# Performance work log

Measured on AMD Instinct MI355X. Metric: run time of the kernel, lower is better.

Reference implementation:

```python
import jax, jax.numpy as jnp
import numpy as np

DIM = 1024
N_HEADS = 8
N_KV_HEADS = 8
Q_C = 128
Q_NOPE = 96
Q_ROPE = 32
KV_C = 128
K_NOPE = 64
K_ROPE = 64
V_HD = 256
EPS = 1e-8
ROPE_THETA = 10000.0


def rms_norm(x, w, eps=EPS):
    return w * x * jax.lax.rsqrt(jnp.mean(x * x, axis=-1, keepdims=True) + eps)


def apply_rope(x, position_ids, head_dim):
    # x: [B, H, S, hd], interleaved even/odd rotation (matches torch module)
    inv_freq = 1.0 / (ROPE_THETA ** (jnp.arange(0, head_dim, 2, dtype=jnp.float32) / head_dim))
    ang = position_ids.astype(jnp.float32)[:, None, :, None] * inv_freq  # [B,1,S,hd/2]
    cos, sin = jnp.cos(ang), jnp.sin(ang)
    xe, xo = x[..., ::2], x[..., 1::2]
    rot = jnp.stack((xe * cos - xo * sin, xe * sin + xo * cos), axis=-1)
    return rot.reshape(x.shape)


def setup_inputs() -> dict:
    key = jax.random.key(0)
    ks = jax.random.split(key, 12)
    B, S = 2, 2048
    s = 0.02
    return {
        "x": jax.random.normal(ks[0], (B, S, DIM), jnp.float32),
        "position_ids": jnp.broadcast_to(jnp.arange(S, dtype=jnp.int32), (B, S)),
        "w_dq_w": jax.random.normal(ks[1], (DIM, Q_C), jnp.float32) * s,
        "w_dq_b": jnp.zeros((Q_C,), jnp.float32),
        "q_norm_w": jnp.ones((Q_C,), jnp.float32),
        "w_uq_qr_w": jax.random.normal(ks[2], (Q_C, N_HEADS * (Q_NOPE + Q_ROPE)), jnp.float32) * s,
        "w_uq_qr_b": jnp.zeros((N_HEADS * (Q_NOPE + Q_ROPE),), jnp.float32),
        "w_dkv_kr_w": jax.random.normal(ks[3], (DIM, KV_C + K_ROPE), jnp.float32) * s,
        "w_dkv_kr_b": jnp.zeros((KV_C + K_ROPE,), jnp.float32),
        "kv_norm_w": jnp.ones((KV_C,), jnp.float32),
        "w_uk_uv_w": jax.random.normal(ks[4], (KV_C, N_KV_HEADS * (K_NOPE + V_HD)), jnp.float32) * s,
        "w_uk_uv_b": jnp.zeros((N_KV_HEADS * (K_NOPE + V_HD),), jnp.float32),
        "w_o_w": jax.random.normal(ks[5], (N_HEADS * V_HD, DIM), jnp.float32) * s,
        "w_o_b": jnp.zeros((DIM,), jnp.float32),
    }


def reference(x, position_ids, w_dq_w, w_dq_b, q_norm_w, w_uq_qr_w, w_uq_qr_b,
              w_dkv_kr_w, w_dkv_kr_b, kv_norm_w, w_uk_uv_w, w_uk_uv_b, w_o_w, w_o_b):
    B, S, _ = x.shape
    # --- Q path: compress -> norm -> up-project, split nope/rope ---
    cq = rms_norm(x @ w_dq_w + w_dq_b, q_norm_w)                     # [B,S,Qc]
    q = cq @ w_uq_qr_w + w_uq_qr_b                                   # [B,S,H*(96+32)]
    q_nope, q_rope = jnp.split(q, [N_HEADS * Q_NOPE], axis=-1)
    q_nope = q_nope.reshape(B, S, N_HEADS, Q_NOPE).transpose(0, 2, 1, 3)
    q_rope = q_rope.reshape(B, S, N_HEADS, Q_ROPE).transpose(0, 2, 1, 3)
    q_rope = apply_rope(q_rope, position_ids, Q_ROPE)
    q_states = jnp.concatenate((q_nope, q_rope), axis=-1)            # [B,H,S,128]
    # --- KV path: compress + shared rope key ---
    ckv_kr = x @ w_dkv_kr_w + w_dkv_kr_b
    ckv, k_rope = jnp.split(ckv_kr, [KV_C], axis=-1)
    ckv = rms_norm(ckv, kv_norm_w)                                   # [B,S,KVc]
    k_rope = apply_rope(k_rope[:, None, :, :], position_ids, K_ROPE) # [B,1,S,64]
    kv = ckv @ w_uk_uv_w + w_uk_uv_b                                 # [B,S,KVh*(64+256)]
    k_nope, v = jnp.split(kv, [N_KV_HEADS * K_NOPE], axis=-1)
    k_nope = k_nope.reshape(B, S, N_KV_HEADS, K_NOPE).transpose(0, 2, 1, 3)
    k_rope = jnp.broadcast_to(k_rope, (B, N_KV_HEADS, S, K_ROPE))
    k_states = jnp.concatenate((k_nope, k_rope), axis=-1)            # [B,KVh,S,128]
    v_states = v.reshape(B, S, N_KV_HEADS, V_HD).transpose(0, 2, 1, 3)
    # gqa_factor = n_heads // n_kv_heads = 1 -> repeat is a no-op
    # --- SDPA (no mask), scale = 1/sqrt(q head dim) ---
    scale = 1.0 / jnp.sqrt(jnp.float32(Q_NOPE + Q_ROPE))
    scores = jnp.einsum("bhqd,bhkd->bhqk", q_states, k_states) * scale
    probs = jax.nn.softmax(scores, axis=-1)
    attn = jnp.einsum("bhqk,bhkd->bhqd", probs, v_states)            # [B,H,S,256]
    attn = attn.transpose(0, 2, 1, 3).reshape(B, S, N_HEADS * V_HD)
    return attn @ w_o_w + w_o_b
```

## Files before the change

kernel.cpp:

```cpp
#include <hip/hip_runtime.h>
#include <hip/hip_bf16.h>
#include <stdint.h>

typedef unsigned short u16;
typedef short short8 __attribute__((ext_vector_type(8)));
typedef float floatx4 __attribute__((ext_vector_type(4)));

#define S_LEN 2048
#define NB 2
#define NH 8
#define R_TOK (NB * S_LEN)

#define L2_THETA 13.287712379549449f
#define QSCALE (0.08838834764831845f * 1.4426950408889634f)

__device__ inline u16 f2bf(float f) {
  union { float f; uint32_t u; } x; x.f = f;
  uint32_t r = (x.u + 0x7fffu + ((x.u >> 16) & 1u)) >> 16;
  return (u16)r;
}
__device__ inline float bf2f(u16 h) {
  union { uint32_t u; float f; } x; x.u = ((uint32_t)h) << 16;
  return x.f;
}
__device__ inline floatx4 mfma16(short8 a, short8 b, floatx4 c) {
  return __builtin_amdgcn_mfma_f32_16x16x32_bf16(a, b, c, 0, 0, 0);
}
__device__ inline uint32_t pkbf(float a, float b) {
  union { __hip_bfloat162 h; uint32_t u; } c;
  c.h = __float22bfloat162_rn(make_float2(a, b));
  return c.u;
}
__device__ __forceinline__ void cp16(const void* g, const void* l) {
  __builtin_amdgcn_global_load_lds(
      (const __attribute__((address_space(1))) uint32_t*)(uintptr_t)g,
      (__attribute__((address_space(3))) uint32_t*)(uintptr_t)l, 16, 0, 0);
}

__global__ __launch_bounds__(256) void k_prep(
    const float* __restrict__ x, u16* __restrict__ xbf,
    const float* __restrict__ wdq, const float* __restrict__ wdkv, u16* __restrict__ waT,
    const float* __restrict__ wuq, u16* __restrict__ wQT,
    const float* __restrict__ wukv, u16* __restrict__ wKVT,
    const float* __restrict__ wo, u16* __restrict__ wOT,
    const float* __restrict__ bdq, const float* __restrict__ bdkv,
    float* __restrict__ biasA) {
  __shared__ u16 tile[32][33];
  const int s = blockIdx.x, tid = threadIdx.x;
  const int tx = tid & 31, ty = tid >> 5;
  if (s < 4096) {
    int i = s * 256 + tid;
    float4 v = ((const float4*)x)[i];
    ushort4 o;
    o.x = f2bf(v.x); o.y = f2bf(v.y); o.z = f2bf(v.z); o.w = f2bf(v.w);
    ((ushort4*)xbf)[i] = o;
  } else if (s < 4416) {
    int t = s - 4096, bx = t % 10, by = t / 10;
    int c0 = bx * 32, r0 = by * 32;
#pragma unroll
    for (int i = 0; i < 4; ++i) {
      int r = r0 + ty + i * 8, c = c0 + tx;
      float v = (c < 128) ? wdq[(size_t)r * 128 + c] : wdkv[(size_t)r * 192 + (c - 128)];
      tile[ty + i * 8][tx] = f2bf(v);
    }
    __syncthreads();
#pragma unroll
    for (int i = 0; i < 4; ++i)
      waT[(size_t)(c0 + ty + i * 8) * 1024 + r0 + tx] = tile[tx][ty + i * 8];
  } else {
    const float* in; u16* out; int R, C, bx, by;
    if (s < 4544) { int t = s - 4416; in = wuq; out = wQT; R = 128; C = 1024; bx = t & 31; by = t >> 5; }
    else if (s < 4864) { int t = s - 4544; in = wukv; out = wKVT; R = 128; C = 2560; bx = t % 80; by = t / 80; }
    else if (s < 6912) { int t = s - 4864; in = wo; out = wOT; R = 2048; C = 1024; bx = t & 31; by = t >> 5; }
    else {
      if (tid < 320) biasA[tid] = (tid < 128) ? bdq[tid] : bdkv[tid - 128];
      return;
    }
    int c0 = bx * 32, r0 = by * 32;
#pragma unroll
    for (int i = 0; i < 4; ++i)
      tile[ty + i * 8][tx] = f2bf(in[(size_t)(r0 + ty + i * 8) * C + c0 + tx]);
    __syncthreads();
#pragma unroll
    for (int i = 0; i < 4; ++i)
      out[(size_t)(c0 + ty + i * 8) * R + r0 + tx] = tile[tx][ty + i * 8];
  }
}

template <int OUT_BF>
__global__ __launch_bounds__(256) void k_gemm_bt(const u16* __restrict__ A,
                                                 const u16* __restrict__ BT,
                                                 const float* __restrict__ bias,
                                                 void* __restrict__ Cout,
                                                 int M, int N, int K) {
  __shared__ __align__(16) u16 Alds[2][128 * 32];
  __shared__ __align__(16) u16 Blds[2][128 * 32];
  const int tid = threadIdx.x;
  const int wave = tid >> 6, lane = tid & 63;
  const int lane15 = lane & 15, quad = lane >> 4;
  const int m0 = blockIdx.y * 128, n0 = blockIdx.x * 128;
  const int mw = (wave & 1) * 64, nw = (wave >> 1) * 64;

  floatx4 acc[4][4];
#pragma unroll
  for (int a = 0; a < 4; ++a)
#pragma unroll
    for (int b = 0; b < 4; ++b) acc[a][b] = (floatx4){0.f, 0.f, 0.f, 0.f};

  const int srow = wave * 32 + (lane >> 2);
  const int scol = (lane & 3) * 8;

  auto stage = [&](int k0, int buf) {
    const u16* ga = A + (size_t)(m0 + srow) * K + k0 + scol;
    cp16(ga, Alds[buf] + srow * 32 + scol);
    cp16(ga + (size_t)16 * K, Alds[buf] + (srow + 16) * 32 + scol);
    const u16* gb = BT + (size_t)(n0 + srow) * K + k0 + scol;
    cp16(gb, Blds[buf] + srow * 32 + scol);
    cp16(gb + (size_t)16 * K, Blds[buf] + (srow + 16) * 32 + scol);
  };

  stage(0, 0);
  int cur = 0;
  for (int k0 = 0; k0 < K; k0 += 32) {
    __syncthreads();
    if (k0 + 32 < K) stage(k0 + 32, cur ^ 1);
    short8 af[4], bf[4];
#pragma unroll
    for (int im = 0; im < 4; ++im)
      af[im] = *(const short8*)&Alds[cur][(mw + im * 16 + lane15) * 32 + quad * 8];
#pragma unroll
    for (int in = 0; in < 4; ++in)
      bf[in] = *(const short8*)&Blds[cur][(nw + in * 16 + lane15) * 32 + quad * 8];
#pragma unroll
    for (int im = 0; im < 4; ++im)
#pragma unroll
      for (int in = 0; in < 4; ++in) acc[im][in] = mfma16(af[im], bf[in], acc[im][in]);
    cur ^= 1;
  }

#pragma unroll
  for (int im = 0; im < 4; ++im)
#pragma unroll
    for (int in = 0; in < 4; ++in)
#pragma unroll
      for (int r = 0; r < 4; ++r) {
        int row = m0 + mw + im * 16 + quad * 4 + r;
        int col = n0 + nw + in * 16 + lane15;
        if (col < N) {
          float v = acc[im][in][r] + bias[col];
          if (OUT_BF)
            ((u16*)Cout)[(size_t)row * N + col] = f2bf(v);
          else
            ((float*)Cout)[(size_t)row * N + col] = v;
        }
      }
}

__global__ void k_stagea(const float* __restrict__ t0, const float* __restrict__ qnw,
                         const float* __restrict__ kvnw, const int* __restrict__ pos_ids,
                         u16* __restrict__ cq, u16* __restrict__ ckv,
                         u16* __restrict__ krope) {
  int r = blockIdx.x, tid = threadIdx.x;
  const float* row = t0 + (size_t)r * 320;
  float a = row[tid];
  float b = row[128 + tid];
  float sa = a * a, sb = b * b;
#pragma unroll
  for (int d = 1; d < 64; d <<= 1) {
    sa += __shfl_xor(sa, d);
    sb += __shfl_xor(sb, d);
  }
  __shared__ float red[4];
  if ((tid & 63) == 0) { red[(tid >> 6) * 2] = sa; red[(tid >> 6) * 2 + 1] = sb; }
  __syncthreads();
  sa = red[0] + red[2];
  sb = red[1] + red[3];
  float ra = rsqrtf(sa * (1.0f / 128.0f) + 1e-8f);
  float rb = rsqrtf(sb * (1.0f / 128.0f) + 1e-8f);
  cq[(size_t)r * 128 + tid] = f2bf(qnw[tid] * a * ra);
  ckv[(size_t)r * 128 + tid] = f2bf(kvnw[tid] * b * rb);
  if (tid < 32) {
    float xe = row[256 + 2 * tid], xo = row[256 + 2 * tid + 1];
    float p = (float)pos_ids[r];
    float freq = exp2f(-(2.0f * tid / 64.0f) * L2_THETA);
    float ang = p * freq;
    float c = cosf(ang), s = sinf(ang);
    krope[(size_t)r * 64 + 2 * tid] = f2bf(xe * c - xo * s);
    krope[(size_t)r * 64 + 2 * tid + 1] = f2bf(xe * s + xo * c);
  }
}

__global__ void k_stageb(const u16* __restrict__ q, const int* __restrict__ pos_ids,
                         u16* __restrict__ qstates) {
  int r = blockIdx.x, tid = threadIdx.x;
  int b = r >> 11, s = r & (S_LEN - 1);
  float p = (float)pos_ids[r];
#pragma unroll
  for (int i = 0; i < 4; ++i) {
    int idx = tid + i * 256;
    int h = idx >> 7, d = idx & 127;
    float val;
    if (d < 96) {
      val = bf2f(q[(size_t)r * 1024 + h * 96 + d]);
    } else {
      int j = d - 96, pr = j >> 1;
      float xe = bf2f(q[(size_t)r * 1024 + 768 + h * 32 + 2 * pr]);
      float xo = bf2f(q[(size_t)r * 1024 + 768 + h * 32 + 2 * pr + 1]);
      float freq = exp2f(-(2.0f * pr / 32.0f) * L2_THETA);
      float ang = p * freq;
      float c = cosf(ang), sn = sinf(ang);
      val = (j & 1) ? (xe * sn + xo * c) : (xe * c - xo * sn);
    }
    qstates[((size_t)(b * NH + h) * S_LEN + s) * 128 + d] = f2bf(val * QSCALE);
  }
}

__global__ __launch_bounds__(256) void k_vt(const u16* __restrict__ kvb, u16* __restrict__ vT) {
  __shared__ u16 tile[64][40];
  const int nx = blockIdx.x;
  const int sy = blockIdx.y;
  const int pz = blockIdx.z;
  const int b = pz >> 3, h = pz & 7;
  const int tid = threadIdx.x;
  const int n0 = nx * 32, s0 = sy * 64;
  {
    int rr = tid >> 2, cc = (tid & 3) * 8;
    const u16* src = kvb + ((size_t)(b * S_LEN + s0 + rr)) * 2560 + 512 + h * 256 + n0 + cc;
    *(short8*)&tile[rr][cc] = *(const short8*)src;
  }
  __syncthreads();
#pragma unroll
  for (int j = 0; j < 2; ++j) {
    int e = tid * 2 + j;
    int n = e >> 4, a = e & 15;
    int sb = 32 * (a >> 3) + 16 * (a & 1) + 4 * ((a >> 1) & 3);
    ushort4 o;
    o.x = tile[sb][n]; o.y = tile[sb + 1][n]; o.z = tile[sb + 2][n]; o.w = tile[sb + 3][n];
    *(ushort4*)&vT[((size_t)(pz * 256 + n0 + n)) * 2048 + s0 + a * 4] = o;
  }
}

__global__ __launch_bounds__(512) void k_attn(const u16* __restrict__ qstates,
                                              const u16* __restrict__ kv,
                                              const u16* __restrict__ krope,
                                              const u16* __restrict__ vT,
                                              u16* __restrict__ attn_out) {
  const int pair = blockIdx.x;
  const int qblk = blockIdx.y;
  const int b = pair >> 3, h = pair & 7;
  const int tid = threadIdx.x;
  const int wave = tid >> 6, lane = tid & 63;
  const int lane15 = lane & 15, quad = lane >> 4;
  const int w4 = wave & 3, half = wave >> 2;

  __shared__ __align__(16) u16 Klds[2][64 * 128];
  __shared__ __align__(16) u16 Vlds[2][256 * 64];

  const int qrow0 = qblk * 128 + wave * 16;
  short8 qfrag[4];
  {
    const u16* qb = qstates + ((size_t)(b * NH + h) * S_LEN + qrow0 + lane15) * 128 + quad * 8;
#pragma unroll
    for (int c = 0; c < 4; ++c) qfrag[c] = *(const short8*)(qb + c * 32);
  }

  floatx4 o_acc[16];
#pragma unroll
  for (int g = 0; g < 16; ++g) o_acc[g] = (floatx4){0.f, 0.f, 0.f, 0.f};
  float m_i = -1e30f;
  float l_i = 0.f;

  const int kbase = (quad * 16 + lane15) * 8;
  int vo0[4], vo1[4];
#pragma unroll
  for (int ph = 0; ph < 4; ++ph) {
    int n = ph * 16 + lane15;
    int sw = (n ^ (n >> 3)) & 7;
    vo0[ph] = n * 64 + ((quad ^ sw) & 7) * 8;
    vo1[ph] = n * 64 + (((quad | 4) ^ sw) & 7) * 8;
  }

  const u16* kp[2];
  int kstr[2];
  int kdst[2];
#pragma unroll
  for (int j = 0; j < 2; ++j) {
    int u = half * 8 + j * 4 + quad;
    const u16* base;
    int str;
    if (u < 8) { base = kv + h * 64 + u * 8; str = 2560; }
    else { base = krope + (u - 8) * 8; str = 64; }
    kp[j] = base + (size_t)(b * S_LEN + w4 * 16 + lane15) * str;
    kstr[j] = str;
    kdst[j] = (w4 * 256 + (half * 2 + j) * 64 + lane) * 8;
  }
  const int vn6 = tid >> 3, vsl = tid & 7;
  const u16* vp[4];
#pragma unroll
  for (int oi = 0; oi < 4; ++oi) {
    int n = oi * 64 + vn6;
    int u = vsl ^ ((n ^ (n >> 3)) & 7);
    vp[oi] = vT + ((size_t)pair * 256 + n) * 2048 + u * 8;
  }

  auto issueK = [&](int buf) {
#pragma unroll
    for (int j = 0; j < 2; ++j) {
      cp16(kp[j], &Klds[buf][kdst[j]]);
      kp[j] += (size_t)64 * kstr[j];
    }
  };
  auto issueV = [&](int buf) {
#pragma unroll
    for (int oi = 0; oi < 4; ++oi) {
      cp16(vp[oi], &Vlds[buf][(oi * 512 + tid) * 8]);
      vp[oi] += 64;
    }
  };

  issueK(0);
  issueV(0);
  asm volatile("s_waitcnt vmcnt(0)" ::: "memory");
  __builtin_amdgcn_sched_barrier(0);
  __builtin_amdgcn_s_barrier();

  int cur = 0;
  for (int ch = 0; ch < S_LEN / 64; ++ch) {
    if (ch + 1 < S_LEN / 64) {
      issueK(cur ^ 1);
      issueV(cur ^ 1);
    }

    floatx4 st[4];
#pragma unroll
    for (int t = 0; t < 4; ++t) st[t] = (floatx4){0.f, 0.f, 0.f, 0.f};
    __builtin_amdgcn_s_setprio(1);
#pragma unroll
    for (int c = 0; c < 4; ++c) {
      short8 qf = qfrag[c];
#pragma unroll
      for (int t = 0; t < 4; ++t) {
        short8 kf = *(const short8*)&Klds[cur][kbase + (t * 16 + c * 4) * 128];
        st[t] = mfma16(kf, qf, st[t]);
      }
    }
    __builtin_amdgcn_s_setprio(0);

    float mloc = st[0][0];
#pragma unroll
    for (int t = 0; t < 4; ++t)
#pragma unroll
      for (int r = 0; r < 4; ++r) mloc = fmaxf(mloc, st[t][r]);
    mloc = fmaxf(mloc, __shfl_xor(mloc, 16));
    mloc = fmaxf(mloc, __shfl_xor(mloc, 32));

    const bool resc = __any(mloc > m_i + 8.0f);
    const float mref = resc ? fmaxf(m_i, mloc) : m_i;

    float rs = 0.f;
    union { short8 s; uint4 u; } a01, a23;
    {
      float p0, p1, p2, p3;
      p0 = exp2f(st[0][0] - mref); p1 = exp2f(st[0][1] - mref);
      p2 = exp2f(st[0][2] - mref); p3 = exp2f(st[0][3] - mref);
      rs += (p0 + p1) + (p2 + p3);
      a01.u.x = pkbf(p0, p1); a01.u.y = pkbf(p2, p3);
      p0 = exp2f(st[1][0] - mref); p1 = exp2f(st[1][1] - mref);
      p2 = exp2f(st[1][2] - mref); p3 = exp2f(st[1][3] - mref);
      rs += (p0 + p1) + (p2 + p3);
      a01.u.z = pkbf(p0, p1); a01.u.w = pkbf(p2, p3);
      p0 = exp2f(st[2][0] - mref); p1 = exp2f(st[2][1] - mref);
      p2 = exp2f(st[2][2] - mref); p3 = exp2f(st[2][3] - mref);
      rs += (p0 + p1) + (p2 + p3);
      a23.u.x = pkbf(p0, p1); a23.u.y = pkbf(p2, p3);
      p0 = exp2f(st[3][0] - mref); p1 = exp2f(st[3][1] - mref);
      p2 = exp2f(st[3][2] - mref); p3 = exp2f(st[3][3] - mref);
      rs += (p0 + p1) + (p2 + p3);
      a23.u.z = pkbf(p0, p1); a23.u.w = pkbf(p2, p3);
    }

    if (resc) {
      float alpha = exp2f(m_i - mref);
      m_i = mref;
      l_i = l_i * alpha + rs;
      float al[4];
#pragma unroll
      for (int r = 0; r < 4; ++r) al[r] = __shfl(alpha, quad * 4 + r, 16);
#pragma unroll
      for (int g = 0; g < 16; ++g) {
        o_acc[g][0] *= al[0]; o_acc[g][1] *= al[1];
        o_acc[g][2] *= al[2]; o_acc[g][3] *= al[3];
      }
    } else {
      l_i += rs;
    }

    __builtin_amdgcn_s_setprio(1);
#pragma unroll
    for (int g = 0; g < 16; ++g) {
      short8 b01 = *(const short8*)&Vlds[cur][vo0[g & 3] + (g >> 2) * 4096];
      short8 b23 = *(const short8*)&Vlds[cur][vo1[g & 3] + (g >> 2) * 4096];
      floatx4 o = o_acc[g];
      o = mfma16(a01.s, b01, o);
      o = mfma16(a23.s, b23, o);
      o_acc[g] = o;
    }
    __builtin_amdgcn_s_setprio(0);

    asm volatile("s_waitcnt vmcnt(0)" ::: "memory");
    __builtin_amdgcn_sched_barrier(0);
    __builtin_amdgcn_s_barrier();
    cur ^= 1;
  }

  float lsum = l_i;
  lsum += __shfl_xor(lsum, 16);
  lsum += __shfl_xor(lsum, 32);
  float rl = 1.0f / lsum;
  float linv[4];
#pragma unroll
  for (int r = 0; r < 4; ++r) linv[r] = __shfl(rl, quad * 4 + r, 16);
#pragma unroll
  for (int g = 0; g < 16; ++g) {
#pragma unroll
    for (int r = 0; r < 4; ++r) {
      int row = qrow0 + quad * 4 + r;
      int col = h * 256 + g * 16 + lane15;
      attn_out[((size_t)b * S_LEN + row) * 2048 + col] = f2bf(o_acc[g][r] * linv[r]);
    }
  }
}

extern "C" void kernel_launch(void* const* d_in, const int* in_sizes, int n_in,
                              void* d_out, int out_size, void* d_ws, size_t ws_size,
                              hipStream_t stream) {
  const float* x = (const float*)d_in[0];
  const int* pos = (const int*)d_in[1];
  const float* wdq = (const float*)d_in[2];
  const float* bdq = (const float*)d_in[3];
  const float* qnw = (const float*)d_in[4];
  const float* wuq = (const float*)d_in[5];
  const float* buq = (const float*)d_in[6];
  const float* wdkv = (const float*)d_in[7];
  const float* bdkv = (const float*)d_in[8];
  const float* kvnw = (const float*)d_in[9];
  const float* wukv = (const float*)d_in[10];
  const float* bukv = (const float*)d_in[11];
  const float* wo = (const float*)d_in[12];
  const float* bo = (const float*)d_in[13];
  float* out = (float*)d_out;

  char* ws = (char*)d_ws;
  size_t off = 0;
  auto alloc = [&](size_t bytes) {
    char* p = ws + off;
    off += (bytes + 255) & ~(size_t)255;
    return p;
  };
  u16* xbf = (u16*)alloc((size_t)R_TOK * 1024 * 2);
  float* t0 = (float*)alloc((size_t)R_TOK * 320 * 4);
  u16* qout = (u16*)alloc((size_t)R_TOK * 1024 * 2);
  u16* vT = (u16*)d_ws;
  u16* waT = (u16*)alloc((size_t)384 * 1024 * 2);
  float* biasA = (float*)alloc(320 * 4);
  u16* wQT = (u16*)alloc((size_t)1024 * 128 * 2);
  u16* wKVT = (u16*)alloc((size_t)2560 * 128 * 2);
  u16* wOT = (u16*)alloc((size_t)1024 * 2048 * 2);
  u16* cq = (u16*)alloc((size_t)R_TOK * 128 * 2);
  u16* ckv = (u16*)alloc((size_t)R_TOK * 128 * 2);
  u16* krope = (u16*)alloc((size_t)R_TOK * 64 * 2);
  u16* qst = (u16*)alloc((size_t)R_TOK * 1024 * 2);
  u16* kvb = (u16*)alloc((size_t)R_TOK * 2560 * 2);
  u16* attnb = (u16*)alloc((size_t)R_TOK * 2048 * 2);
  (void)ws_size; (void)n_in; (void)in_sizes; (void)out_size;

  k_prep<<<6913, 256, 0, stream>>>(x, xbf, wdq, wdkv, waT, wuq, wQT, wukv, wKVT, wo, wOT,
                                   bdq, bdkv, biasA);

  k_gemm_bt<0><<<dim3(3, 32), 256, 0, stream>>>(xbf, waT, biasA, t0, R_TOK, 320, 1024);
  k_stagea<<<R_TOK, 128, 0, stream>>>(t0, qnw, kvnw, pos, cq, ckv, krope);
  k_gemm_bt<1><<<dim3(8, 32), 256, 0, stream>>>(cq, wQT, buq, qout, R_TOK, 1024, 128);
  k_stageb<<<R_TOK, 256, 0, stream>>>(qout, pos, qst);
  k_gemm_bt<1><<<dim3(20, 32), 256, 0, stream>>>(ckv, wKVT, bukv, kvb, R_TOK, 2560, 128);
  k_vt<<<dim3(8, 32, 16), 256, 0, stream>>>(kvb, vT);
  k_attn<<<dim3(16, 16), 512, 0, stream>>>(qst, kvb, krope, vT, attnb);
  k_gemm_bt<0><<<dim3(8, 32), 256, 0, stream>>>(attnb, wOT, bo, out, R_TOK, 1024, 2048);
}
```

Measured before the change: 275.0 us.

## Split attention waves into query-pair by V-half tiles for operand reuse

Each wave now handles two 16-row query slices and half of the 256-wide V output instead of one 16-row slice over all 256 columns. Each K fragment read from LDS feeds two MFMAs and each V fragment feeds two, roughly halving LDS read traffic per MFMA. The cost is that QK^T scores and softmax are computed twice, once in each V-half wave. Launch bounds also request 2 blocks per CU, which constrains registers; with 512-thread blocks and 64 KB LDS each, that target may also be tight on shared memory.

```diff
diff --git a/kernel.cpp b/kernel.cpp
--- a/kernel.cpp
+++ b/kernel.cpp
@@ -240,35 +240,40 @@
   }
 }
 
-__global__ __launch_bounds__(512) void k_attn(const u16* __restrict__ qstates,
-                                              const u16* __restrict__ kv,
-                                              const u16* __restrict__ krope,
-                                              const u16* __restrict__ vT,
-                                              u16* __restrict__ attn_out) {
+__global__ __launch_bounds__(512, 2) void k_attn(const u16* __restrict__ qstates,
+                                                 const u16* __restrict__ kv,
+                                                 const u16* __restrict__ krope,
+                                                 const u16* __restrict__ vT,
+                                                 u16* __restrict__ attn_out) {
   const int pair = blockIdx.x;
   const int qblk = blockIdx.y;
   const int b = pair >> 3, h = pair & 7;
   const int tid = threadIdx.x;
   const int wave = tid >> 6, lane = tid & 63;
   const int lane15 = lane & 15, quad = lane >> 4;
-  const int w4 = wave & 3, half = wave >> 2;
+  const int qg = wave & 3;
+  const int nh = wave >> 2;
 
   __shared__ __align__(16) u16 Klds[2][64 * 128];
   __shared__ __align__(16) u16 Vlds[2][256 * 64];
 
-  const int qrow0 = qblk * 128 + wave * 16;
-  short8 qfrag[4];
-  {
-    const u16* qb = qstates + ((size_t)(b * NH + h) * S_LEN + qrow0 + lane15) * 128 + quad * 8;
-#pragma unroll
-    for (int c = 0; c < 4; ++c) qfrag[c] = *(const short8*)(qb + c * 32);
-  }
-
-  floatx4 o_acc[16];
-#pragma unroll
-  for (int g = 0; g < 16; ++g) o_acc[g] = (floatx4){0.f, 0.f, 0.f, 0.f};
-  float m_i = -1e30f;
-  float l_i = 0.f;
+  const int qrow0 = qblk * 128 + qg * 32;
+  short8 qfrag[2][4];
+#pragma unroll
+  for (int s = 0; s < 2; ++s) {
+    const u16* qb =
+        qstates + ((size_t)(b * NH + h) * S_LEN + qrow0 + s * 16 + lane15) * 128 + quad * 8;
+#pragma unroll
+    for (int c = 0; c < 4; ++c) qfrag[s][c] = *(const short8*)(qb + c * 32);
+  }
+
+  floatx4 o_acc[2][8];
+#pragma unroll
+  for (int s = 0; s < 2; ++s)
+#pragma unroll
+    for (int g = 0; g < 8; ++g) o_acc[s][g] = (floatx4){0.f, 0.f, 0.f, 0.f};
+  float m_i[2] = {-1e30f, -1e30f};
+  float l_i[2] = {0.f, 0.f};
 
   const int kbase = (quad * 16 + lane15) * 8;
   int vo0[4], vo1[4];
@@ -276,8 +281,8 @@
   for (int ph = 0; ph < 4; ++ph) {
     int n = ph * 16 + lane15;
     int sw = (n ^ (n >> 3)) & 7;
-    vo0[ph] = n * 64 + ((quad ^ sw) & 7) * 8;
-    vo1[ph] = n * 64 + (((quad | 4) ^ sw) & 7) * 8;
+    vo0[ph] = nh * 8192 + n * 64 + ((quad ^ sw) & 7) * 8;
+    vo1[ph] = nh * 8192 + n * 64 + (((quad | 4) ^ sw) & 7) * 8;
   }
 
   const u16* kp[2];
@@ -285,14 +290,14 @@
   int kdst[2];
 #pragma unroll
   for (int j = 0; j < 2; ++j) {
-    int u = half * 8 + j * 4 + quad;
+    int u = nh * 8 + j * 4 + quad;
     const u16* base;
     int str;
     if (u < 8) { base = kv + h * 64 + u * 8; str = 2560; }
     else { base = krope + (u - 8) * 8; str = 64; }
-    kp[j] = base + (size_t)(b * S_LEN + w4 * 16 + lane15) * str;
+    kp[j] = base + (size_t)(b * S_LEN + qg * 16 + lane15) * str;
     kstr[j] = str;
-    kdst[j] = (w4 * 256 + (half * 2 + j) * 64 + lane) * 8;
+    kdst[j] = (qg * 256 + (nh * 2 + j) * 64 + lane) * 8;
   }
   const int vn6 = tid >> 3, vsl = tid & 7;
   const u16* vp[4];
@@ -331,79 +336,84 @@
       issueV(cur ^ 1);
     }
 
-    floatx4 st[4];
-#pragma unroll
-    for (int t = 0; t < 4; ++t) st[t] = (floatx4){0.f, 0.f, 0.f, 0.f};
+    floatx4 st[2][4];
+#pragma unroll
+    for (int s = 0; s < 2; ++s)
+#pragma unroll
+      for (int t = 0; t < 4; ++t) st[s][t] = (floatx4){0.f, 0.f, 0.f, 0.f};
     __builtin_amdgcn_s_setprio(1);
 #pragma unroll
     for (int c = 0; c < 4; ++c) {
-      short8 qf = qfrag[c];
 #pragma unroll
       for (int t = 0; t < 4; ++t) {
         short8 kf = *(const short8*)&Klds[cur][kbase + (t * 16 + c * 4) * 128];
-        st[t] = mfma16(kf, qf, st[t]);
+        st[0][t] = mfma16(kf, qfrag[0][c], st[0][t]);
+        st[1][t] = mfma16(kf, qfrag[1][c], st[1][t]);
       }
     }
     __builtin_amdgcn_s_setprio(0);
 
-    float mloc = st[0][0];
-#pragma unroll
-    for (int t = 0; t < 4; ++t)
-#pragma unroll
-      for (int r = 0; r < 4; ++r) mloc = fmaxf(mloc, st[t][r]);
-    mloc = fmaxf(mloc, __shfl_xor(mloc, 16));
-    mloc = fmaxf(mloc, __shfl_xor(mloc, 32));
-
-    const bool resc = __any(mloc > m_i + 8.0f);
-    const float mref = resc ? fmaxf(m_i, mloc) : m_i;
-
-    float rs = 0.f;
-    union { short8 s; uint4 u; } a01, a23;
-    {
-      float p0, p1, p2, p3;
-      p0 = exp2f(st[0][0] - mref); p1 = exp2f(st[0][1] - mref);
-      p2 = exp2f(st[0][2] - mref); p3 = exp2f(st[0][3] - mref);
-      rs += (p0 + p1) + (p2 + p3);
-      a01.u.x = pkbf(p0, p1); a01.u.y = pkbf(p2, p3);
-      p0 = exp2f(st[1][0] - mref); p1 = exp2f(st[1][1] - mref);
-      p2 = exp2f(st[1][2] - mref); p3 = exp2f(st[1][3] - mref);
-      rs += (p0 + p1) + (p2 + p3);
-      a01.u.z = pkbf(p0, p1); a01.u.w = pkbf(p2, p3);
-      p0 = exp2f(st[2][0] - mref); p1 = exp2f(st[2][1] - mref);
-      p2 = exp2f(st[2][2] - mref); p3 = exp2f(st[2][3] - mref);
-      rs += (p0 + p1) + (p2 + p3);
-      a23.u.x = pkbf(p0, p1); a23.u.y = pkbf(p2, p3);
-      p0 = exp2f(st[3][0] - mref); p1 = exp2f(st[3][1] - mref);
-      p2 = exp2f(st[3][2] - mref); p3 = exp2f(st[3][3] - mref);
-      rs += (p0 + p1) + (p2 + p3);
-      a23.u.z = pkbf(p0, p1); a23.u.w = pkbf(p2, p3);
-    }
-
-    if (resc) {
-      float alpha = exp2f(m_i - mref);
-      m_i = mref;
-      l_i = l_i * alpha + rs;
-      float al[4];
-#pragma unroll
-      for (int r = 0; r < 4; ++r) al[r] = __shfl(alpha, quad * 4 + r, 16);
-#pragma unroll
-      for (int g = 0; g < 16; ++g) {
-        o_acc[g][0] *= al[0]; o_acc[g][1] *= al[1];
-        o_acc[g][2] *= al[2]; o_acc[g][3] *= al[3];
+    union { short8 s; uint4 u; } a01[2], a23[2];
+#pragma unroll
+    for (int s = 0; s < 2; ++s) {
+      float mloc = st[s][0][0];
+#pragma unroll
+      for (int t = 0; t < 4; ++t)
+#pragma unroll
+        for (int r = 0; r < 4; ++r) mloc = fmaxf(mloc, st[s][t][r]);
+      mloc = fmaxf(mloc, __shfl_xor(mloc, 16));
+      mloc = fmaxf(mloc, __shfl_xor(mloc, 32));
+
+      const bool resc = __any(mloc > m_i[s] + 8.0f);
+      const float mref = resc ? fmaxf(m_i[s], mloc) : m_i[s];
+
+      float rs = 0.f;
+      {
+        float p0, p1, p2, p3;
+        p0 = exp2f(st[s][0][0] - mref); p1 = exp2f(st[s][0][1] - mref);
+        p2 = exp2f(st[s][0][2] - mref); p3 = exp2f(st[s][0][3] - mref);
+        rs += (p0 + p1) + (p2 + p3);
+        a01[s].u.x = pkbf(p0, p1); a01[s].u.y = pkbf(p2, p3);
+        p0 = exp2f(st[s][1][0] - mref); p1 = exp2f(st[s][1][1] - mref);
+        p2 = exp2f(st[s][1][2] - mref); p3 = exp2f(st[s][1][3] - mref);
+        rs += (p0 + p1) + (p2 + p3);
+        a01[s].u.z = pkbf(p0, p1); a01[s].u.w = pkbf(p2, p3);
+        p0 = exp2f(st[s][2][0] - mref); p1 = exp2f(st[s][2][1] - mref);
+        p2 = exp2f(st[s][2][2] - mref); p3 = exp2f(st[s][2][3] - mref);
+        rs += (p0 + p1) + (p2 + p3);
+        a23[s].u.x = pkbf(p0, p1); a23[s].u.y = pkbf(p2, p3);
+        p0 = exp2f(st[s][3][0] - mref); p1 = exp2f(st[s][3][1] - mref);
+        p2 = exp2f(st[s][3][2] - mref); p3 = exp2f(st[s][3][3] - mref);
+        rs += (p0 + p1) + (p2 + p3);
+        a23[s].u.z = pkbf(p0, p1); a23[s].u.w = pkbf(p2, p3);
       }
-    } else {
-      l_i += rs;
+
+      if (resc) {
+        float alpha = exp2f(m_i[s] - mref);
+        m_i[s] = mref;
+        l_i[s] = l_i[s] * alpha + rs;
+        float al[4];
+#pragma unroll
+        for (int r = 0; r < 4; ++r) al[r] = __shfl(alpha, quad * 4 + r, 16);
+#pragma unroll
+        for (int g = 0; g < 8; ++g) {
+          o_acc[s][g][0] *= al[0]; o_acc[s][g][1] *= al[1];
+          o_acc[s][g][2] *= al[2]; o_acc[s][g][3] *= al[3];
+        }
+      } else {
+        l_i[s] += rs;
+      }
     }
 
     __builtin_amdgcn_s_setprio(1);
 #pragma unroll
-    for (int g = 0; g < 16; ++g) {
+    for (int g = 0; g < 8; ++g) {
       short8 b01 = *(const short8*)&Vlds[cur][vo0[g & 3] + (g >> 2) * 4096];
       short8 b23 = *(const short8*)&Vlds[cur][vo1[g & 3] + (g >> 2) * 4096];
-      floatx4 o = o_acc[g];
-      o = mfma16(a01.s, b01, o);
-      o = mfma16(a23.s, b23, o);
-      o_acc[g] = o;
+      o_acc[0][g] = mfma16(a01[0].s, b01, o_acc[0][g]);
+      o_acc[1][g] = mfma16(a01[1].s, b01, o_acc[1][g]);
+      o_acc[0][g] = mfma16(a23[0].s, b23, o_acc[0][g]);
+      o_acc[1][g] = mfma16(a23[1].s, b23, o_acc[1][g]);
     }
     __builtin_amdgcn_s_setprio(0);
 
@@ -413,20 +423,23 @@
     cur ^= 1;
   }
 
-  float lsum = l_i;
-  lsum += __shfl_xor(lsum, 16);
-  lsum += __shfl_xor(lsum, 32);
-  float rl = 1.0f / lsum;
-  float linv[4];
-#pragma unroll
-  for (int r = 0; r < 4; ++r) linv[r] = __shfl(rl, quad * 4 + r, 16);
-#pragma unroll
-  for (int g = 0; g < 16; ++g) {
-#pragma unroll
-    for (int r = 0; r < 4; ++r) {
-      int row = qrow0 + quad * 4 + r;
-      int col = h * 256 + g * 16 + lane15;
-      attn_out[((size_t)b * S_LEN + row) * 2048 + col] = f2bf(o_acc[g][r] * linv[r]);
+#pragma unroll
+  for (int s = 0; s < 2; ++s) {
+    float lsum = l_i[s];
+    lsum += __shfl_xor(lsum, 16);
+    lsum += __shfl_xor(lsum, 32);
+    float rl = 1.0f / lsum;
+    float linv[4];
+#pragma unroll
+    for (int r = 0; r < 4; ++r) linv[r] = __shfl(rl, quad * 4 + r, 16);
+#pragma unroll
+    for (int g = 0; g < 8; ++g) {
+#pragma unroll
+      for (int r = 0; r < 4; ++r) {
+        int row = qrow0 + s * 16 + quad * 4 + r;
+        int col = h * 256 + nh * 128 + g * 16 + lane15;
+        attn_out[((size_t)b * S_LEN + row) * 2048 + col] = f2bf(o_acc[s][g][r] * linv[r]);
+      }
     }
   }
 }
```

New measurement: 297.6 us. +8.2%, slower.

## Fuse q rope/scatter and V transpose into up-projection GEMM epilogues

Applied to the files above, without the earlier changes.

The q up-projection GEMM now writes directly into the per-head qstates layout, applying bias, RoPE (pairing lanes through a shuffle) and the softmax scale in its epilogue, so the separate k_stageb pass and the qout round trip go away. The kv up-projection GEMM writes k_nope rows into kvb as before, but scatters the V columns straight into the permuted transposed vT layout, which removes the k_vt transpose kernel. This saves two launches and the intermediate global traffic. In exchange the epilogue stores are scattered and less coalesced.

```diff
diff --git a/kernel.cpp b/kernel.cpp
--- a/kernel.cpp
+++ b/kernel.cpp
@@ -156,6 +156,178 @@
       }
 }
 
+__global__ __launch_bounds__(256) void k_gemm_q(const u16* __restrict__ A,
+                                                const u16* __restrict__ BT,
+                                                const float* __restrict__ bias,
+                                                const int* __restrict__ pos_ids,
+                                                u16* __restrict__ qstates) {
+  const int K = 128;
+  __shared__ __align__(16) u16 Alds[2][128 * 32];
+  __shared__ __align__(16) u16 Blds[2][128 * 32];
+  const int tid = threadIdx.x;
+  const int wave = tid >> 6, lane = tid & 63;
+  const int lane15 = lane & 15, quad = lane >> 4;
+  const int m0 = blockIdx.y * 128, n0 = blockIdx.x * 128;
+  const int mw = (wave & 1) * 64, nw = (wave >> 1) * 64;
+
+  floatx4 acc[4][4];
+#pragma unroll
+  for (int a = 0; a < 4; ++a)
+#pragma unroll
+    for (int b = 0; b < 4; ++b) acc[a][b] = (floatx4){0.f, 0.f, 0.f, 0.f};
+
+  const int srow = wave * 32 + (lane >> 2);
+  const int scol = (lane & 3) * 8;
+  auto stage = [&](int k0, int buf) {
+    const u16* ga = A + (size_t)(m0 + srow) * K + k0 + scol;
+    cp16(ga, Alds[buf] + srow * 32 + scol);
+    cp16(ga + (size_t)16 * K, Alds[buf] + (srow + 16) * 32 + scol);
+    const u16* gb = BT + (size_t)(n0 + srow) * K + k0 + scol;
+    cp16(gb, Blds[buf] + srow * 32 + scol);
+    cp16(gb + (size_t)16 * K, Blds[buf] + (srow + 16) * 32 + scol);
+  };
+
+  stage(0, 0);
+  int cur = 0;
+  for (int k0 = 0; k0 < K; k0 += 32) {
+    __syncthreads();
+    if (k0 + 32 < K) stage(k0 + 32, cur ^ 1);
+    short8 af[4], bf[4];
+#pragma unroll
+    for (int im = 0; im < 4; ++im)
+      af[im] = *(const short8*)&Alds[cur][(mw + im * 16 + lane15) * 32 + quad * 8];
+#pragma unroll
+    for (int in = 0; in < 4; ++in)
+      bf[in] = *(const short8*)&Blds[cur][(nw + in * 16 + lane15) * 32 + quad * 8];
+#pragma unroll
+    for (int im = 0; im < 4; ++im)
+#pragma unroll
+      for (int in = 0; in < 4; ++in) acc[im][in] = mfma16(af[im], bf[in], acc[im][in]);
+    cur ^= 1;
+  }
+
+  const bool ropeblk = (n0 >= 768);
+#pragma unroll
+  for (int in = 0; in < 4; ++in) {
+    const int col = n0 + nw + in * 16 + lane15;
+#pragma unroll
+    for (int im = 0; im < 4; ++im) {
+      if (!ropeblk) {
+        const int h = col / 96, d = col - h * 96;
+#pragma unroll
+        for (int r = 0; r < 4; ++r) {
+          int row = m0 + mw + im * 16 + quad * 4 + r;
+          int b = row >> 11, s = row & (S_LEN - 1);
+          float v = acc[im][in][r] + bias[col];
+          qstates[((size_t)(b * NH + h) * S_LEN + s) * 128 + d] = f2bf(v * QSCALE);
+        }
+      } else {
+        const int j = (col - 768) & 31, h = (col - 768) >> 5, pr = j >> 1;
+        const float freq = exp2f(-(2.0f * pr / 32.0f) * L2_THETA);
+#pragma unroll
+        for (int r = 0; r < 4; ++r) {
+          int row = m0 + mw + im * 16 + quad * 4 + r;
+          int b = row >> 11, s = row & (S_LEN - 1);
+          float v = acc[im][in][r] + bias[col];
+          float vp = __shfl_xor(v, 1);
+          float xe = (lane & 1) ? vp : v;
+          float xo = (lane & 1) ? v : vp;
+          float p = (float)pos_ids[row];
+          float ang = p * freq;
+          float c = cosf(ang), sn = sinf(ang);
+          float val = (j & 1) ? (xe * sn + xo * c) : (xe * c - xo * sn);
+          qstates[((size_t)(b * NH + h) * S_LEN + s) * 128 + 96 + j] = f2bf(val * QSCALE);
+        }
+      }
+    }
+  }
+}
+
+__global__ __launch_bounds__(256) void k_gemm_kv(const u16* __restrict__ A,
+                                                 const u16* __restrict__ BT,
+                                                 const float* __restrict__ bias,
+                                                 u16* __restrict__ kvb,
+                                                 u16* __restrict__ vT) {
+  const int K = 128, N = 2560;
+  __shared__ __align__(16) u16 Alds[2][128 * 32];
+  __shared__ __align__(16) u16 Blds[2][128 * 32];
+  const int tid = threadIdx.x;
+  const int wave = tid >> 6, lane = tid & 63;
+  const int lane15 = lane & 15, quad = lane >> 4;
+  const int m0 = blockIdx.y * 128, n0 = blockIdx.x * 128;
+  const int mw = (wave & 1) * 64, nw = (wave >> 1) * 64;
+
+  floatx4 acc[4][4];
+#pragma unroll
+  for (int a = 0; a < 4; ++a)
+#pragma unroll
+    for (int b = 0; b < 4; ++b) acc[a][b] = (floatx4){0.f, 0.f, 0.f, 0.f};
+
+  const int srow = wave * 32 + (lane >> 2);
+  const int scol = (lane & 3) * 8;
+  auto stage = [&](int k0, int buf) {
+    const u16* ga = A + (size_t)(m0 + srow) * K + k0 + scol;
+    cp16(ga, Alds[buf] + srow * 32 + scol);
+    cp16(ga + (size_t)16 * K, Alds[buf] + (srow + 16) * 32 + scol);
+    const u16* gb = BT + (size_t)(n0 + srow) * K + k0 + scol;
+    cp16(gb, Blds[buf] + srow * 32 + scol);
+    cp16(gb + (size_t)16 * K, Blds[buf] + (srow + 16) * 32 + scol);
+  };
+
+  stage(0, 0);
+  int cur = 0;
+  for (int k0 = 0; k0 < K; k0 += 32) {
+    __syncthreads();
+    if (k0 + 32 < K) stage(k0 + 32, cur ^ 1);
+    short8 af[4], bf[4];
+#pragma unroll
+    for (int im = 0; im < 4; ++im)
+      af[im] = *(const short8*)&Alds[cur][(mw + im * 16 + lane15) * 32 + quad * 8];
+#pragma unroll
+    for (int in = 0; in < 4; ++in)
+      bf[in] = *(const short8*)&Blds[cur][(nw + in * 16 + lane15) * 32 + quad * 8];
+#pragma unroll
+    for (int im = 0; im < 4; ++im)
+#pragma unroll
+      for (int in = 0; in < 4; ++in) acc[im][in] = mfma16(af[im], bf[in], acc[im][in]);
+    cur ^= 1;
+  }
+
+  if (n0 < 512) {
+#pragma unroll
+    for (int im = 0; im < 4; ++im)
+#pragma unroll
+      for (int in = 0; in < 4; ++in)
+#pragma unroll
+        for (int r = 0; r < 4; ++r) {
+          int row = m0 + mw + im * 16 + quad * 4 + r;
+          int col = n0 + nw + in * 16 + lane15;
+          kvb[(size_t)row * N + col] = f2bf(acc[im][in][r] + bias[col]);
+        }
+  } else {
+#pragma unroll
+    for (int im = 0; im < 4; ++im) {
+      const int row0 = m0 + mw + im * 16 + quad * 4;
+      const int b = row0 >> 11, srow0 = row0 & (S_LEN - 1);
+      const int sc = srow0 & ~63, bb = (srow0 & 63) >> 2;
+      const int a = (bb & 8) | (((bb >> 1) & 1) << 2) | ((bb & 1) << 1) | ((bb >> 2) & 1);
+#pragma unroll
+      for (int in = 0; in < 4; ++in) {
+        const int col = n0 + nw + in * 16 + lane15;
+        const int c2 = col - 512;
+        const int hv = c2 >> 8, n = c2 & 255;
+        const float bv = bias[col];
+        ushort4 o;
+        o.x = f2bf(acc[im][in][0] + bv);
+        o.y = f2bf(acc[im][in][1] + bv);
+        o.z = f2bf(acc[im][in][2] + bv);
+        o.w = f2bf(acc[im][in][3] + bv);
+        *(ushort4*)&vT[((size_t)((b * NH + hv) * 256 + n)) * 2048 + sc + a * 4] = o;
+      }
+    }
+  }
+}
+
 __global__ void k_stagea(const float* __restrict__ t0, const float* __restrict__ qnw,
                          const float* __restrict__ kvnw, const int* __restrict__ pos_ids,
                          u16* __restrict__ cq, u16* __restrict__ ckv,
@@ -187,56 +359,6 @@
     float c = cosf(ang), s = sinf(ang);
     krope[(size_t)r * 64 + 2 * tid] = f2bf(xe * c - xo * s);
     krope[(size_t)r * 64 + 2 * tid + 1] = f2bf(xe * s + xo * c);
-  }
-}
-
-__global__ void k_stageb(const u16* __restrict__ q, const int* __restrict__ pos_ids,
-                         u16* __restrict__ qstates) {
-  int r = blockIdx.x, tid = threadIdx.x;
-  int b = r >> 11, s = r & (S_LEN - 1);
-  float p = (float)pos_ids[r];
-#pragma unroll
-  for (int i = 0; i < 4; ++i) {
-    int idx = tid + i * 256;
-    int h = idx >> 7, d = idx & 127;
-    float val;
-    if (d < 96) {
-      val = bf2f(q[(size_t)r * 1024 + h * 96 + d]);
-    } else {
-      int j = d - 96, pr = j >> 1;
-      float xe = bf2f(q[(size_t)r * 1024 + 768 + h * 32 + 2 * pr]);
-      float xo = bf2f(q[(size_t)r * 1024 + 768 + h * 32 + 2 * pr + 1]);
-      float freq = exp2f(-(2.0f * pr / 32.0f) * L2_THETA);
-      float ang = p * freq;
-      float c = cosf(ang), sn = sinf(ang);
-      val = (j & 1) ? (xe * sn + xo * c) : (xe * c - xo * sn);
-    }
-    qstates[((size_t)(b * NH + h) * S_LEN + s) * 128 + d] = f2bf(val * QSCALE);
-  }
-}
-
-__global__ __launch_bounds__(256) void k_vt(const u16* __restrict__ kvb, u16* __restrict__ vT) {
-  __shared__ u16 tile[64][40];
-  const int nx = blockIdx.x;
-  const int sy = blockIdx.y;
-  const int pz = blockIdx.z;
-  const int b = pz >> 3, h = pz & 7;
-  const int tid = threadIdx.x;
-  const int n0 = nx * 32, s0 = sy * 64;
-  {
-    int rr = tid >> 2, cc = (tid & 3) * 8;
-    const u16* src = kvb + ((size_t)(b * S_LEN + s0 + rr)) * 2560 + 512 + h * 256 + n0 + cc;
-    *(short8*)&tile[rr][cc] = *(const short8*)src;
-  }
-  __syncthreads();
-#pragma unroll
-  for (int j = 0; j < 2; ++j) {
-    int e = tid * 2 + j;
-    int n = e >> 4, a = e & 15;
-    int sb = 32 * (a >> 3) + 16 * (a & 1) + 4 * ((a >> 1) & 3);
-    ushort4 o;
-    o.x = tile[sb][n]; o.y = tile[sb + 1][n]; o.z = tile[sb + 2][n]; o.w = tile[sb + 3][n];
-    *(ushort4*)&vT[((size_t)(pz * 256 + n0 + n)) * 2048 + s0 + a * 4] = o;
   }
 }
 
@@ -472,17 +594,15 @@
   u16* qst = (u16*)alloc((size_t)R_TOK * 1024 * 2);
   u16* kvb = (u16*)alloc((size_t)R_TOK * 2560 * 2);
   u16* attnb = (u16*)alloc((size_t)R_TOK * 2048 * 2);
-  (void)ws_size; (void)n_in; (void)in_sizes; (void)out_size;
+  (void)ws_size; (void)n_in; (void)in_sizes; (void)out_size; (void)qout;
 
   k_prep<<<6913, 256, 0, stream>>>(x, xbf, wdq, wdkv, waT, wuq, wQT, wukv, wKVT, wo, wOT,
                                    bdq, bdkv, biasA);
 
   k_gemm_bt<0><<<dim3(3, 32), 256, 0, stream>>>(xbf, waT, biasA, t0, R_TOK, 320, 1024);
   k_stagea<<<R_TOK, 128, 0, stream>>>(t0, qnw, kvnw, pos, cq, ckv, krope);
-  k_gemm_bt<1><<<dim3(8, 32), 256, 0, stream>>>(cq, wQT, buq, qout, R_TOK, 1024, 128);
-  k_stageb<<<R_TOK, 256, 0, stream>>>(qout, pos, qst);
-  k_gemm_bt<1><<<dim3(20, 32), 256, 0, stream>>>(ckv, wKVT, bukv, kvb, R_TOK, 2560, 128);
-  k_vt<<<dim3(8, 32, 16), 256, 0, stream>>>(kvb, vT);
+  k_gemm_q<<<dim3(8, 32), 256, 0, stream>>>(cq, wQT, buq, pos, qst);
+  k_gemm_kv<<<dim3(20, 32), 256, 0, stream>>>(ckv, wKVT, bukv, kvb, vT);
   k_attn<<<dim3(16, 16), 512, 0, stream>>>(qst, kvb, krope, vT, attnb);
   k_gemm_bt<0><<<dim3(8, 32), 256, 0, stream>>>(attnb, wOT, bo, out, R_TOK, 1024, 2048);
 }
```

Result: slower. 284.3 us (+3.4%).
